# Kernel optimization log

Hardware: AMD Instinct MI355X
Metric: run time of the kernel (lower is better)

## Reference

```python
import jax, jax.numpy as jnp
import numpy as np

B, S, D = 2, 2048, 1024
H = 16
HD = D // H  # head dim 64


def setup_inputs() -> dict:
    key = jax.random.key(0)
    ks = jax.random.split(key, 7)
    queries = jax.random.normal(ks[0], (B, S, D), dtype=jnp.float32)
    keys = jax.random.normal(ks[1], (B, S, D), dtype=jnp.float32)
    values = jax.random.normal(ks[2], (B, S, D), dtype=jnp.float32)
    scale = 1.0 / np.sqrt(D)
    Wq = jax.random.normal(ks[3], (D, D), dtype=jnp.float32) * scale
    Wk = jax.random.normal(ks[4], (D, D), dtype=jnp.float32) * scale
    Wv = jax.random.normal(ks[5], (D, D), dtype=jnp.float32) * scale
    Wo = jax.random.normal(ks[6], (D, D), dtype=jnp.float32) * scale
    return {"queries": queries, "keys": keys, "values": values,
            "Wq": Wq, "Wk": Wk, "Wv": Wv, "Wo": Wo}


def _split_heads(x):
    # [B,S,D] -> [B,H,S,HD]
    b, s, d = x.shape
    return x.reshape(b, s, H, d // H).transpose(0, 2, 1, 3)


def reference(queries, keys, values, Wq, Wk, Wv, Wo):
    q = _split_heads(queries @ Wq) * (HD ** -0.5)   # [B,H,S,HD]
    k = _split_heads(keys @ Wk)
    v = _split_heads(values @ Wv)
    logits = jnp.einsum('bhqd,bhkd->bhqk', q, k)     # [B,H,S,S]
    weights = jax.nn.softmax(logits, axis=-1)
    ctx = jnp.einsum('bhqk,bhkd->bhqd', weights, v)  # [B,H,S,HD]
    ctx = ctx.transpose(0, 2, 1, 3).reshape(B, S, D)
    return ctx @ Wo
```

## Files before the change

kernel.cpp:

```cpp
#include <hip/hip_runtime.h>
#include <hip/hip_bf16.h>


typedef short s16x8 __attribute__((ext_vector_type(8)));
typedef float f32x4v __attribute__((ext_vector_type(4)));
typedef float f32x16v __attribute__((ext_vector_type(16)));
typedef unsigned int u32x4v __attribute__((ext_vector_type(4)));

__device__ inline unsigned short f2bf(float f) {
    union { float f; unsigned int i; } x; x.f = f;
    unsigned int r = x.i + 0x7FFFu + ((x.i >> 16) & 1u);
    return (unsigned short)(r >> 16);
}
__device__ inline unsigned int pkbf(float lo, float hi) {
    return (unsigned int)f2bf(lo) | ((unsigned int)f2bf(hi) << 16);
}

__device__ inline void gld_lds16(const unsigned short* g, unsigned short* l) {
    __builtin_amdgcn_global_load_lds(
        (const __attribute__((address_space(1))) unsigned int*)(const void*)g,
        (__attribute__((address_space(3))) unsigned int*)(void*)l,
        16, 0, 0);
}

__global__ __launch_bounds__(256)
void cvt3(const float* __restrict__ W0, const float* __restrict__ W1, const float* __restrict__ W2,
          unsigned short* __restrict__ T0, unsigned short* __restrict__ T1, unsigned short* __restrict__ T2) {
    const float* W = (blockIdx.z == 0) ? W0 : (blockIdx.z == 1) ? W1 : W2;
    unsigned short* Wt = (blockIdx.z == 0) ? T0 : (blockIdx.z == 1) ? T1 : T2;
    __shared__ __align__(16) unsigned short Ls[64 * 72];
    const int t = threadIdx.x;
    const int k0 = blockIdx.y * 64, n0 = blockIdx.x * 64;
    const int r = t >> 4, c4 = (t & 15) * 4;
    #pragma unroll
    for (int i = 0; i < 4; ++i) {
        float4 wv = *(const float4*)&W[(size_t)(k0 + r + i * 16) * 1024 + n0 + c4];
        Ls[(c4 + 0) * 72 + r + i * 16] = f2bf(wv.x);
        Ls[(c4 + 1) * 72 + r + i * 16] = f2bf(wv.y);
        Ls[(c4 + 2) * 72 + r + i * 16] = f2bf(wv.z);
        Ls[(c4 + 3) * 72 + r + i * 16] = f2bf(wv.w);
    }
    __syncthreads();
    #pragma unroll
    for (int i = 0; i < 2; ++i) {
        const int p = i * 256 + t;
        const int n = p & 63, kc = p >> 6;
        s16x8 v = *(const s16x8*)&Ls[n * 72 + kc * 8];
        const int gn = n0 + n, k = k0 + kc * 8;
        const size_t g = ((size_t)(gn >> 7) * 128 + (k >> 3)) * 128 + (gn & 127);
        *(s16x8*)&Wt[g * 8] = v;
    }
}

__global__ __launch_bounds__(256, 3)
void gemm_qkv(const float* __restrict__ A0, const float* __restrict__ A1, const float* __restrict__ A2,
              const unsigned short* __restrict__ W0, const unsigned short* __restrict__ W1,
              const unsigned short* __restrict__ W2,
              unsigned short* __restrict__ OQ, unsigned short* __restrict__ OK,
              unsigned short* __restrict__ OV, float scaleQ) {
    const int z = blockIdx.z;
    const float* Av = (z == 0) ? A0 : (z == 1) ? A1 : A2;
    const unsigned short* Bsw = (z == 0) ? W0 : (z == 1) ? W1 : W2;
    const float scale = (z == 0) ? scaleQ : 1.0f;

    __shared__ __align__(16) unsigned short Al[1024 * 8];
    __shared__ __align__(16) unsigned short Bl[1024 * 8];
    const int t = threadIdx.x;
    const int lane = t & 63, w = t >> 6;
    const int ln = lane & 15, qd = lane >> 4;
    const int mw = (w & 1) * 64, nw = (w >> 1) * 64;
    const int m0 = blockIdx.y * 128, n0 = blockIdx.x * 128;

    f32x4v acc[4][4] = {};

    for (int k0 = 0; k0 < 1024; k0 += 64) {
        __syncthreads();
        {
            const size_t gb = ((size_t)(n0 >> 7) * 128 + (k0 >> 3)) * 128;
            #pragma unroll
            for (int j = 0; j < 4; ++j)
                gld_lds16(Bsw + (gb + j * 256 + t) * 8, &Bl[(j * 256 + w * 64) * 8]);
        }
        #pragma unroll
        for (int j = 0; j < 4; ++j) {
            const int p = j * 256 + t;
            const int row = p >> 3, kc = p & 7;
            const float* src = Av + (size_t)(m0 + row) * 1024 + k0 + kc * 8;
            float4 f0 = ((const float4*)src)[0];
            float4 f1 = ((const float4*)src)[1];
            uint4 u;
            u.x = pkbf(f0.x, f0.y); u.y = pkbf(f0.z, f0.w);
            u.z = pkbf(f1.x, f1.y); u.w = pkbf(f1.z, f1.w);
            *(uint4*)&Al[(kc * 128 + (row ^ kc)) * 8] = u;
        }
        __syncthreads();

        #pragma unroll
        for (int kk = 0; kk < 2; ++kk) {
            const int kc = kk * 4 + qd;
            s16x8 a[4], b[4];
            #pragma unroll
            for (int mt = 0; mt < 4; ++mt)
                a[mt] = *(const s16x8*)&Al[(kc * 128 + ((mw + mt * 16 + ln) ^ kc)) * 8];
            #pragma unroll
            for (int nt = 0; nt < 4; ++nt)
                b[nt] = *(const s16x8*)&Bl[(kc * 128 + nw + nt * 16 + ln) * 8];
            #pragma unroll
            for (int mt = 0; mt < 4; ++mt)
                #pragma unroll
                for (int nt = 0; nt < 4; ++nt)
                    acc[mt][nt] = __builtin_amdgcn_mfma_f32_16x16x32_bf16(a[mt], b[nt], acc[mt][nt], 0, 0, 0);
        }
    }

    #pragma unroll
    for (int mt = 0; mt < 4; ++mt)
        #pragma unroll
        for (int nt = 0; nt < 4; ++nt)
            #pragma unroll
            for (int i = 0; i < 4; ++i) {
                const int m = m0 + mw + mt * 16 + qd * 4 + i;
                const int n = n0 + nw + nt * 16 + ln;
                const float v = acc[mt][nt][i] * scale;
                const int bh = (m >> 11) * 16 + (n >> 6), s = m & 2047, hd = n & 63;
                if (z == 0) {
                    OQ[((size_t)bh * 2048 + s) * 64 + hd] = f2bf(v);
                } else if (z == 1) {
                    const size_t g = ((size_t)(bh * 32 + (s >> 6)) * 8 + (hd >> 3)) * 64 + (s & 63);
                    OK[g * 8 + (hd & 7)] = f2bf(v);
                } else {
                    const size_t g = ((size_t)(bh * 32 + (s >> 6)) * 8 + ((s >> 3) & 7)) * 64 + hd;
                    OV[g * 8 + (s & 7)] = f2bf(v);
                }
            }
}

__global__ __launch_bounds__(256, 2)
void gemm_out(const unsigned short* __restrict__ Asw, const unsigned short* __restrict__ Bsw,
              float* __restrict__ outF) {
    __shared__ __align__(16) unsigned short Al[1024 * 8];
    __shared__ __align__(16) unsigned short Bl[512 * 8];
    const int t = threadIdx.x;
    const int lane = t & 63, w = t >> 6;
    const int ln = lane & 15, qd = lane >> 4;
    const int mw = (w & 1) * 64, nw = (w >> 1) * 32;
    const int m0 = blockIdx.y * 128, n0 = blockIdx.x * 64;

    f32x4v acc[4][2] = {};

    for (int k0 = 0; k0 < 1024; k0 += 64) {
        __syncthreads();
        {
            const size_t ga = ((size_t)(m0 >> 7) * 128 + (k0 >> 3)) * 128;
            #pragma unroll
            for (int j = 0; j < 4; ++j)
                gld_lds16(Asw + (ga + j * 256 + t) * 8, &Al[(j * 256 + w * 64) * 8]);
        }
        {
            #pragma unroll
            for (int i = 0; i < 2; ++i) {
                const int c = w * 2 + i;
                const size_t gb = ((size_t)(n0 >> 7) * 128 + (k0 >> 3) + c) * 128 + (n0 & 127) + lane;
                gld_lds16(Bsw + gb * 8, &Bl[(c * 64) * 8]);
            }
        }
        __syncthreads();

        #pragma unroll
        for (int kk = 0; kk < 2; ++kk) {
            const int kc = kk * 4 + qd;
            s16x8 a[4], b[2];
            #pragma unroll
            for (int mt = 0; mt < 4; ++mt)
                a[mt] = *(const s16x8*)&Al[(kc * 128 + mw + mt * 16 + ln) * 8];
            #pragma unroll
            for (int nt = 0; nt < 2; ++nt)
                b[nt] = *(const s16x8*)&Bl[(kc * 64 + nw + nt * 16 + ln) * 8];
            #pragma unroll
            for (int mt = 0; mt < 4; ++mt)
                #pragma unroll
                for (int nt = 0; nt < 2; ++nt)
                    acc[mt][nt] = __builtin_amdgcn_mfma_f32_16x16x32_bf16(a[mt], b[nt], acc[mt][nt], 0, 0, 0);
        }
    }

    #pragma unroll
    for (int mt = 0; mt < 4; ++mt)
        #pragma unroll
        for (int nt = 0; nt < 2; ++nt)
            #pragma unroll
            for (int i = 0; i < 4; ++i) {
                const int m = m0 + mw + mt * 16 + qd * 4 + i;
                const int n = n0 + nw + nt * 16 + ln;
                outF[(size_t)m * 1024 + n] = acc[mt][nt][i];
            }
}

__global__ __launch_bounds__(256, 2)
void fattn(const unsigned short* __restrict__ Q, const unsigned short* __restrict__ Ksw,
           const unsigned short* __restrict__ Vsw, unsigned short* __restrict__ ctx) {
    __shared__ __align__(16) unsigned short Ks2[2][512 * 8];
    __shared__ __align__(16) unsigned short Vs2[2][512 * 8];

    const int t = threadIdx.x, lane = t & 63, w = t >> 6;
    const int l31 = lane & 31, H = lane >> 5;
    const int bh = blockIdx.y, m0 = blockIdx.x * 128;
    const size_t head = (size_t)bh * 2048 * 64;

    s16x8 qf[4];
    #pragma unroll
    for (int kk = 0; kk < 4; ++kk)
        qf[kk] = *(const s16x8*)(Q + head + (size_t)(m0 + w * 32 + l31) * 64 + kk * 16 + H * 8);

    f32x16v accO[2] = {};
    float lsum = 0.f;

    {
        const size_t tb = (size_t)bh * 32 * 512;
        #pragma unroll
        for (int j = 0; j < 2; ++j) {
            gld_lds16(Ksw + (tb + j * 256 + t) * 8, &Ks2[0][(j * 256 + w * 64) * 8]);
            gld_lds16(Vsw + (tb + j * 256 + t) * 8, &Vs2[0][(j * 256 + w * 64) * 8]);
        }
    }

    for (int kt = 0; kt < 32; ++kt) {
        const int cur = kt & 1;
        __syncthreads();
        if (kt + 1 < 32) {
            const size_t tb = ((size_t)bh * 32 + kt + 1) * 512;
            #pragma unroll
            for (int j = 0; j < 2; ++j) {
                gld_lds16(Ksw + (tb + j * 256 + t) * 8, &Ks2[cur ^ 1][(j * 256 + w * 64) * 8]);
                gld_lds16(Vsw + (tb + j * 256 + t) * 8, &Vs2[cur ^ 1][(j * 256 + w * 64) * 8]);
            }
        }

        f32x16v accS[2] = {};
        #pragma unroll
        for (int kk = 0; kk < 4; ++kk)
            #pragma unroll
            for (int mt = 0; mt < 2; ++mt) {
                s16x8 kf = *(const s16x8*)&Ks2[cur][((kk * 2 + H) * 64 + mt * 32 + l31) * 8];
                accS[mt] = __builtin_amdgcn_mfma_f32_32x32x16_bf16(kf, qf[kk], accS[mt], 0, 0, 0);
            }

        u32x4v af[4];
        #pragma unroll
        for (int mt = 0; mt < 2; ++mt) {
            float p[16];
            #pragma unroll
            for (int r = 0; r < 16; ++r) {
                p[r] = exp2f(accS[mt][r]);
                lsum += p[r];
            }
            unsigned int C[8];
            #pragma unroll
            for (int j = 0; j < 8; ++j)
                asm("v_cvt_pk_bf16_f32 %0, %1, %2" : "=v"(C[j]) : "v"(p[2 * j]), "v"(p[2 * j + 1]));
            #pragma unroll
            for (int pp = 0; pp < 2; ++pp) {
                unsigned int x0 = C[4 * pp + 0], y0 = C[4 * pp + 2];
                unsigned int x1 = C[4 * pp + 1], y1 = C[4 * pp + 3];
                asm("v_permlane32_swap_b32 %0, %1" : "+v"(x0), "+v"(y0));
                asm("v_permlane32_swap_b32 %0, %1" : "+v"(x1), "+v"(y1));
                u32x4v a; a.x = x0; a.y = x1; a.z = y0; a.w = y1;
                af[mt * 2 + pp] = a;
            }
        }

        #pragma unroll
        for (int kk2 = 0; kk2 < 4; ++kk2) {
            s16x8 a = __builtin_bit_cast(s16x8, af[kk2]);
            #pragma unroll
            for (int nt = 0; nt < 2; ++nt) {
                s16x8 b = *(const s16x8*)&Vs2[cur][((kk2 * 2 + H) * 64 + nt * 32 + l31) * 8];
                accO[nt] = __builtin_amdgcn_mfma_f32_32x32x16_bf16(a, b, accO[nt], 0, 0, 0);
            }
        }
    }

    lsum += __shfl_xor(lsum, 32, 64);
    const float inv = 1.f / lsum;

    #pragma unroll
    for (int r = 0; r < 16; ++r) {
        const int qloc = (r & 3) + 8 * (r >> 2) + 4 * H;
        const float rinv = __shfl(inv, qloc, 64);
        const int mrow = (bh >> 4) * 2048 + m0 + w * 32 + qloc;
        #pragma unroll
        for (int nt = 0; nt < 2; ++nt) {
            const int k = (bh & 15) * 64 + nt * 32 + l31;
            const size_t g = ((size_t)(mrow >> 7) * 128 + (k >> 3)) * 128 + (mrow & 127);
            ctx[g * 8 + (k & 7)] = f2bf(accO[nt][r] * rinv);
        }
    }
}

extern "C" void kernel_launch(void* const* d_in, const int* in_sizes, int n_in,
                              void* d_out, int out_size, void* d_ws, size_t ws_size,
                              hipStream_t stream) {
    char* ws = (char*)d_ws;
    unsigned short* Qb  = (unsigned short*)(ws);
    unsigned short* Ksw = (unsigned short*)(ws + ((size_t)8 << 20));
    unsigned short* Vsw = (unsigned short*)(ws + ((size_t)16 << 20));
    unsigned short* Wqt = (unsigned short*)(ws + ((size_t)24 << 20));
    unsigned short* Wkt = (unsigned short*)(ws + ((size_t)26 << 20));
    unsigned short* Wvt = (unsigned short*)(ws + ((size_t)28 << 20));
    unsigned short* ctx = (unsigned short*)(ws + ((size_t)24 << 20));
    unsigned short* Wot = (unsigned short*)(ws);

    cvt3<<<dim3(16, 16, 3), 256, 0, stream>>>((const float*)d_in[3], (const float*)d_in[4],
                                              (const float*)d_in[5], Wqt, Wkt, Wvt);

    gemm_qkv<<<dim3(8, 32, 3), 256, 0, stream>>>(
        (const float*)d_in[0], (const float*)d_in[1], (const float*)d_in[2],
        Wqt, Wkt, Wvt, Qb, Ksw, Vsw, 0.125f * 1.44269504f);

    fattn<<<dim3(16, 32), dim3(256), 0, stream>>>(Qb, Ksw, Vsw, ctx);

    cvt3<<<dim3(16, 16, 1), 256, 0, stream>>>((const float*)d_in[6], nullptr, nullptr,
                                              Wot, nullptr, nullptr);

    gemm_out<<<dim3(16, 32), 256, 0, stream>>>(ctx, Wot, (float*)d_out);
}
```

Baseline: 241.5 us.

## Load K/V fragments directly from global into registers, dropping LDS staging

The flash-attention kernel stops staging K and V tiles through double-buffered shared memory with block-wide barriers. Each wave now loads its MFMA operand fragments straight from global memory into registers, prefetching the next K tile into a ping-pong register set while loading V for the current tile. Block IDs are also remapped so that blocks for the same head are spread across groups, and the row-sum is split into four independent accumulators. This removes the LDS traffic and the __syncthreads per tile. In exchange every wave re-reads K and V from global/L2 and register pressure rises, which may hurt occupancy.

```diff
diff --git a/kernel.cpp b/kernel.cpp
--- a/kernel.cpp
+++ b/kernel.cpp
@@ -196,15 +196,69 @@
             }
 }
 
+
+__device__ __forceinline__ void fa_tile(
+        const unsigned short* __restrict__ vt,
+        const unsigned short* __restrict__ kn,
+        const s16x8* kcur, s16x8* knext, const s16x8* qf,
+        f32x16v* accO, float& ls0, float& ls1, float& ls2, float& ls3) {
+    s16x8 vf[8];
+    #pragma unroll
+    for (int u = 0; u < 8; ++u)
+        vf[u] = *(const s16x8*)(vt + (u >> 1) * 1024 + (u & 1) * 256);
+    #pragma unroll
+    for (int u = 0; u < 8; ++u)
+        knext[u] = *(const s16x8*)(kn + (u >> 1) * 1024 + (u & 1) * 256);
+
+    f32x16v accS[2] = {};
+    #pragma unroll
+    for (int kk = 0; kk < 4; ++kk) {
+        accS[0] = __builtin_amdgcn_mfma_f32_32x32x16_bf16(kcur[kk * 2 + 0], qf[kk], accS[0], 0, 0, 0);
+        accS[1] = __builtin_amdgcn_mfma_f32_32x32x16_bf16(kcur[kk * 2 + 1], qf[kk], accS[1], 0, 0, 0);
+    }
+
+    u32x4v af[4];
+    #pragma unroll
+    for (int mt = 0; mt < 2; ++mt) {
+        float p[16];
+        #pragma unroll
+        for (int r = 0; r < 16; ++r)
+            p[r] = exp2f(accS[mt][r]);
+        #pragma unroll
+        for (int r = 0; r < 16; r += 4) {
+            ls0 += p[r + 0]; ls1 += p[r + 1]; ls2 += p[r + 2]; ls3 += p[r + 3];
+        }
+        unsigned int C[8];
+        #pragma unroll
+        for (int j = 0; j < 8; ++j)
+            asm("v_cvt_pk_bf16_f32 %0, %1, %2" : "=v"(C[j]) : "v"(p[2 * j]), "v"(p[2 * j + 1]));
+        #pragma unroll
+        for (int pp = 0; pp < 2; ++pp) {
+            unsigned int x0 = C[4 * pp + 0], y0 = C[4 * pp + 2];
+            unsigned int x1 = C[4 * pp + 1], y1 = C[4 * pp + 3];
+            asm("v_permlane32_swap_b32 %0, %1" : "+v"(x0), "+v"(y0));
+            asm("v_permlane32_swap_b32 %0, %1" : "+v"(x1), "+v"(y1));
+            u32x4v a; a.x = x0; a.y = x1; a.z = y0; a.w = y1;
+            af[mt * 2 + pp] = a;
+        }
+    }
+
+    #pragma unroll
+    for (int kk2 = 0; kk2 < 4; ++kk2) {
+        s16x8 a = __builtin_bit_cast(s16x8, af[kk2]);
+        accO[0] = __builtin_amdgcn_mfma_f32_32x32x16_bf16(a, vf[kk2 * 2 + 0], accO[0], 0, 0, 0);
+        accO[1] = __builtin_amdgcn_mfma_f32_32x32x16_bf16(a, vf[kk2 * 2 + 1], accO[1], 0, 0, 0);
+    }
+}
+
 __global__ __launch_bounds__(256, 2)
 void fattn(const unsigned short* __restrict__ Q, const unsigned short* __restrict__ Ksw,
            const unsigned short* __restrict__ Vsw, unsigned short* __restrict__ ctx) {
-    __shared__ __align__(16) unsigned short Ks2[2][512 * 8];
-    __shared__ __align__(16) unsigned short Vs2[2][512 * 8];
-
     const int t = threadIdx.x, lane = t & 63, w = t >> 6;
     const int l31 = lane & 31, H = lane >> 5;
-    const int bh = blockIdx.y, m0 = blockIdx.x * 128;
+    const int bid = blockIdx.x + (blockIdx.y << 4);
+    const int wid = (bid & 7) * 64 + (bid >> 3);
+    const int bh = wid >> 4, m0 = (wid & 15) * 128;
     const size_t head = (size_t)bh * 2048 * 64;
 
     s16x8 qf[4];
@@ -212,74 +266,27 @@
     for (int kk = 0; kk < 4; ++kk)
         qf[kk] = *(const s16x8*)(Q + head + (size_t)(m0 + w * 32 + l31) * 64 + kk * 16 + H * 8);
 
+    const unsigned short* kb = Ksw + (size_t)bh * 32 * 4096 + H * 512 + l31 * 8;
+    const unsigned short* vb = Vsw + (size_t)bh * 32 * 4096 + H * 512 + l31 * 8;
+
     f32x16v accO[2] = {};
-    float lsum = 0.f;
-
-    {
-        const size_t tb = (size_t)bh * 32 * 512;
-        #pragma unroll
-        for (int j = 0; j < 2; ++j) {
-            gld_lds16(Ksw + (tb + j * 256 + t) * 8, &Ks2[0][(j * 256 + w * 64) * 8]);
-            gld_lds16(Vsw + (tb + j * 256 + t) * 8, &Vs2[0][(j * 256 + w * 64) * 8]);
-        }
-    }
-
-    for (int kt = 0; kt < 32; ++kt) {
-        const int cur = kt & 1;
-        __syncthreads();
-        if (kt + 1 < 32) {
-            const size_t tb = ((size_t)bh * 32 + kt + 1) * 512;
-            #pragma unroll
-            for (int j = 0; j < 2; ++j) {
-                gld_lds16(Ksw + (tb + j * 256 + t) * 8, &Ks2[cur ^ 1][(j * 256 + w * 64) * 8]);
-                gld_lds16(Vsw + (tb + j * 256 + t) * 8, &Vs2[cur ^ 1][(j * 256 + w * 64) * 8]);
-            }
-        }
-
-        f32x16v accS[2] = {};
-        #pragma unroll
-        for (int kk = 0; kk < 4; ++kk)
-            #pragma unroll
-            for (int mt = 0; mt < 2; ++mt) {
-                s16x8 kf = *(const s16x8*)&Ks2[cur][((kk * 2 + H) * 64 + mt * 32 + l31) * 8];
-                accS[mt] = __builtin_amdgcn_mfma_f32_32x32x16_bf16(kf, qf[kk], accS[mt], 0, 0, 0);
-            }
-
-        u32x4v af[4];
-        #pragma unroll
-        for (int mt = 0; mt < 2; ++mt) {
-            float p[16];
-            #pragma unroll
-            for (int r = 0; r < 16; ++r) {
-                p[r] = exp2f(accS[mt][r]);
-                lsum += p[r];
-            }
-            unsigned int C[8];
-            #pragma unroll
-            for (int j = 0; j < 8; ++j)
-                asm("v_cvt_pk_bf16_f32 %0, %1, %2" : "=v"(C[j]) : "v"(p[2 * j]), "v"(p[2 * j + 1]));
-            #pragma unroll
-            for (int pp = 0; pp < 2; ++pp) {
-                unsigned int x0 = C[4 * pp + 0], y0 = C[4 * pp + 2];
-                unsigned int x1 = C[4 * pp + 1], y1 = C[4 * pp + 3];
-                asm("v_permlane32_swap_b32 %0, %1" : "+v"(x0), "+v"(y0));
-                asm("v_permlane32_swap_b32 %0, %1" : "+v"(x1), "+v"(y1));
-                u32x4v a; a.x = x0; a.y = x1; a.z = y0; a.w = y1;
-                af[mt * 2 + pp] = a;
-            }
-        }
-
-        #pragma unroll
-        for (int kk2 = 0; kk2 < 4; ++kk2) {
-            s16x8 a = __builtin_bit_cast(s16x8, af[kk2]);
-            #pragma unroll
-            for (int nt = 0; nt < 2; ++nt) {
-                s16x8 b = *(const s16x8*)&Vs2[cur][((kk2 * 2 + H) * 64 + nt * 32 + l31) * 8];
-                accO[nt] = __builtin_amdgcn_mfma_f32_32x32x16_bf16(a, b, accO[nt], 0, 0, 0);
-            }
-        }
-    }
-
+    float ls0 = 0.f, ls1 = 0.f, ls2 = 0.f, ls3 = 0.f;
+
+    s16x8 kfA[8], kfB[8];
+    #pragma unroll
+    for (int u = 0; u < 8; ++u)
+        kfA[u] = *(const s16x8*)(kb + (u >> 1) * 1024 + (u & 1) * 256);
+
+    for (int kt2 = 0; kt2 < 16; ++kt2) {
+        fa_tile(vb + (size_t)(2 * kt2) * 4096,
+                kb + (size_t)((2 * kt2 + 1) & 31) * 4096,
+                kfA, kfB, qf, accO, ls0, ls1, ls2, ls3);
+        fa_tile(vb + (size_t)(2 * kt2 + 1) * 4096,
+                kb + (size_t)((2 * kt2 + 2) & 31) * 4096,
+                kfB, kfA, qf, accO, ls0, ls1, ls2, ls3);
+    }
+
+    float lsum = (ls0 + ls1) + (ls2 + ls3);
     lsum += __shfl_xor(lsum, 32, 64);
     const float inv = 1.f / lsum;
 
```

Measured after the change: 278.2 us. 15.2% more time.

## Triple-buffer K/V tiles in attention with explicit vmcnt waits and block swizzle

Applied to the files above, without the earlier changes.

Replaces the double-buffered K/V LDS pipeline with a three-stage ring that prefetches two tiles ahead. It also replaces __syncthreads with a partial s_waitcnt vmcnt(4) plus raw s_barrier, so only the oldest tile's loads are awaited. The flat grid index is remapped so that blocks spread across heads, and the row-sum is split into four independent accumulators to shorten the dependency chain. The cost is 50% more LDS per block, which could limit occupancy. It also relies on hand-written vmcnt counts that must exactly match the number of outstanding loads.

```diff
diff --git a/kernel.cpp b/kernel.cpp
--- a/kernel.cpp
+++ b/kernel.cpp
@@ -196,90 +196,118 @@
             }
 }
 
+
+__device__ __forceinline__ void fa_compute(
+        const unsigned short* Ksb, const unsigned short* Vsb,
+        const int H, const int l31, const s16x8* qf,
+        f32x16v* accO, float& ls0, float& ls1, float& ls2, float& ls3) {
+    f32x16v accS[2] = {};
+    #pragma unroll
+    for (int kk = 0; kk < 4; ++kk) {
+        s16x8 kf0 = *(const s16x8*)&Ksb[((kk * 2 + H) * 64 + l31) * 8];
+        s16x8 kf1 = *(const s16x8*)&Ksb[((kk * 2 + H) * 64 + 32 + l31) * 8];
+        accS[0] = __builtin_amdgcn_mfma_f32_32x32x16_bf16(kf0, qf[kk], accS[0], 0, 0, 0);
+        accS[1] = __builtin_amdgcn_mfma_f32_32x32x16_bf16(kf1, qf[kk], accS[1], 0, 0, 0);
+    }
+
+    u32x4v af[4];
+    #pragma unroll
+    for (int mt = 0; mt < 2; ++mt) {
+        float p[16];
+        #pragma unroll
+        for (int r = 0; r < 16; ++r)
+            p[r] = exp2f(accS[mt][r]);
+        #pragma unroll
+        for (int r = 0; r < 16; r += 4) {
+            ls0 += p[r + 0]; ls1 += p[r + 1]; ls2 += p[r + 2]; ls3 += p[r + 3];
+        }
+        unsigned int C[8];
+        #pragma unroll
+        for (int j = 0; j < 8; ++j)
+            asm("v_cvt_pk_bf16_f32 %0, %1, %2" : "=v"(C[j]) : "v"(p[2 * j]), "v"(p[2 * j + 1]));
+        #pragma unroll
+        for (int pp = 0; pp < 2; ++pp) {
+            unsigned int x0 = C[4 * pp + 0], y0 = C[4 * pp + 2];
+            unsigned int x1 = C[4 * pp + 1], y1 = C[4 * pp + 3];
+            asm("v_permlane32_swap_b32 %0, %1" : "+v"(x0), "+v"(y0));
+            asm("v_permlane32_swap_b32 %0, %1" : "+v"(x1), "+v"(y1));
+            u32x4v a; a.x = x0; a.y = x1; a.z = y0; a.w = y1;
+            af[mt * 2 + pp] = a;
+        }
+    }
+
+    #pragma unroll
+    for (int kk2 = 0; kk2 < 4; ++kk2) {
+        s16x8 a = __builtin_bit_cast(s16x8, af[kk2]);
+        s16x8 vf0 = *(const s16x8*)&Vsb[((kk2 * 2 + H) * 64 + l31) * 8];
+        s16x8 vf1 = *(const s16x8*)&Vsb[((kk2 * 2 + H) * 64 + 32 + l31) * 8];
+        accO[0] = __builtin_amdgcn_mfma_f32_32x32x16_bf16(a, vf0, accO[0], 0, 0, 0);
+        accO[1] = __builtin_amdgcn_mfma_f32_32x32x16_bf16(a, vf1, accO[1], 0, 0, 0);
+    }
+}
+
 __global__ __launch_bounds__(256, 2)
 void fattn(const unsigned short* __restrict__ Q, const unsigned short* __restrict__ Ksw,
            const unsigned short* __restrict__ Vsw, unsigned short* __restrict__ ctx) {
-    __shared__ __align__(16) unsigned short Ks2[2][512 * 8];
-    __shared__ __align__(16) unsigned short Vs2[2][512 * 8];
+    __shared__ __align__(16) unsigned short Ks3[3][512 * 8];
+    __shared__ __align__(16) unsigned short Vs3[3][512 * 8];
 
     const int t = threadIdx.x, lane = t & 63, w = t >> 6;
     const int l31 = lane & 31, H = lane >> 5;
-    const int bh = blockIdx.y, m0 = blockIdx.x * 128;
+    const int bid = blockIdx.x + (blockIdx.y << 4);
+    const int wid = (bid & 7) * 64 + (bid >> 3);
+    const int bh = wid >> 4, m0 = (wid & 15) * 128;
     const size_t head = (size_t)bh * 2048 * 64;
 
     s16x8 qf[4];
     #pragma unroll
     for (int kk = 0; kk < 4; ++kk)
         qf[kk] = *(const s16x8*)(Q + head + (size_t)(m0 + w * 32 + l31) * 64 + kk * 16 + H * 8);
+    asm volatile("s_waitcnt vmcnt(0)" ::: "memory");
+    #pragma unroll
+    for (int kk = 0; kk < 4; ++kk) {
+        u32x4v q = __builtin_bit_cast(u32x4v, qf[kk]);
+        asm volatile("" : "+v"(q.x), "+v"(q.y), "+v"(q.z), "+v"(q.w));
+        qf[kk] = __builtin_bit_cast(s16x8, q);
+    }
+
+    const size_t tb = (size_t)bh * 32 * 512;
+    {
+        #pragma unroll
+        for (int kt = 0; kt < 2; ++kt)
+            #pragma unroll
+            for (int j = 0; j < 2; ++j) {
+                gld_lds16(Ksw + (tb + kt * 512 + j * 256 + t) * 8, &Ks3[kt][(j * 256 + w * 64) * 8]);
+                gld_lds16(Vsw + (tb + kt * 512 + j * 256 + t) * 8, &Vs3[kt][(j * 256 + w * 64) * 8]);
+            }
+    }
 
     f32x16v accO[2] = {};
-    float lsum = 0.f;
-
-    {
-        const size_t tb = (size_t)bh * 32 * 512;
-        #pragma unroll
-        for (int j = 0; j < 2; ++j) {
-            gld_lds16(Ksw + (tb + j * 256 + t) * 8, &Ks2[0][(j * 256 + w * 64) * 8]);
-            gld_lds16(Vsw + (tb + j * 256 + t) * 8, &Vs2[0][(j * 256 + w * 64) * 8]);
-        }
-    }
-
-    for (int kt = 0; kt < 32; ++kt) {
-        const int cur = kt & 1;
-        __syncthreads();
-        if (kt + 1 < 32) {
-            const size_t tb = ((size_t)bh * 32 + kt + 1) * 512;
+    float ls0 = 0.f, ls1 = 0.f, ls2 = 0.f, ls3 = 0.f;
+
+    int cur = 0;
+    for (int kt = 0; kt < 31; ++kt) {
+        asm volatile("s_waitcnt vmcnt(4)" ::: "memory");
+        __builtin_amdgcn_s_barrier();
+        asm volatile("" ::: "memory");
+        if (kt < 30) {
+            const int ib = (cur == 0) ? 2 : cur - 1;
+            const size_t tbn = tb + (size_t)(kt + 2) * 512;
             #pragma unroll
             for (int j = 0; j < 2; ++j) {
-                gld_lds16(Ksw + (tb + j * 256 + t) * 8, &Ks2[cur ^ 1][(j * 256 + w * 64) * 8]);
-                gld_lds16(Vsw + (tb + j * 256 + t) * 8, &Vs2[cur ^ 1][(j * 256 + w * 64) * 8]);
-            }
-        }
-
-        f32x16v accS[2] = {};
-        #pragma unroll
-        for (int kk = 0; kk < 4; ++kk)
-            #pragma unroll
-            for (int mt = 0; mt < 2; ++mt) {
-                s16x8 kf = *(const s16x8*)&Ks2[cur][((kk * 2 + H) * 64 + mt * 32 + l31) * 8];
-                accS[mt] = __builtin_amdgcn_mfma_f32_32x32x16_bf16(kf, qf[kk], accS[mt], 0, 0, 0);
-            }
-
-        u32x4v af[4];
-        #pragma unroll
-        for (int mt = 0; mt < 2; ++mt) {
-            float p[16];
-            #pragma unroll
-            for (int r = 0; r < 16; ++r) {
-                p[r] = exp2f(accS[mt][r]);
-                lsum += p[r];
-            }
-            unsigned int C[8];
-            #pragma unroll
-            for (int j = 0; j < 8; ++j)
-                asm("v_cvt_pk_bf16_f32 %0, %1, %2" : "=v"(C[j]) : "v"(p[2 * j]), "v"(p[2 * j + 1]));
-            #pragma unroll
-            for (int pp = 0; pp < 2; ++pp) {
-                unsigned int x0 = C[4 * pp + 0], y0 = C[4 * pp + 2];
-                unsigned int x1 = C[4 * pp + 1], y1 = C[4 * pp + 3];
-                asm("v_permlane32_swap_b32 %0, %1" : "+v"(x0), "+v"(y0));
-                asm("v_permlane32_swap_b32 %0, %1" : "+v"(x1), "+v"(y1));
-                u32x4v a; a.x = x0; a.y = x1; a.z = y0; a.w = y1;
-                af[mt * 2 + pp] = a;
-            }
-        }
-
-        #pragma unroll
-        for (int kk2 = 0; kk2 < 4; ++kk2) {
-            s16x8 a = __builtin_bit_cast(s16x8, af[kk2]);
-            #pragma unroll
-            for (int nt = 0; nt < 2; ++nt) {
-                s16x8 b = *(const s16x8*)&Vs2[cur][((kk2 * 2 + H) * 64 + nt * 32 + l31) * 8];
-                accO[nt] = __builtin_amdgcn_mfma_f32_32x32x16_bf16(a, b, accO[nt], 0, 0, 0);
-            }
-        }
-    }
-
+                gld_lds16(Ksw + (tbn + j * 256 + t) * 8, &Ks3[ib][(j * 256 + w * 64) * 8]);
+                gld_lds16(Vsw + (tbn + j * 256 + t) * 8, &Vs3[ib][(j * 256 + w * 64) * 8]);
+            }
+        }
+        fa_compute(Ks3[cur], Vs3[cur], H, l31, qf, accO, ls0, ls1, ls2, ls3);
+        cur = (cur == 2) ? 0 : cur + 1;
+    }
+    asm volatile("s_waitcnt vmcnt(0)" ::: "memory");
+    __builtin_amdgcn_s_barrier();
+    asm volatile("" ::: "memory");
+    fa_compute(Ks3[cur], Vs3[cur], H, l31, qf, accO, ls0, ls1, ls2, ls3);
+
+    float lsum = (ls0 + ls1) + (ls2 + ls3);
     lsum += __shfl_xor(lsum, 32, 64);
     const float inv = 1.f / lsum;
 
```

After: 241.3 us. No clear change (-0.1%).
